# Performance work log

Hardware: AMD Instinct MI355X
Metric: run time of the kernel (lower is better)

The kernel has to match this reference:

```python
import jax, jax.numpy as jnp
import numpy as np

N_CHANNELS = 1024
N_HEADS = 16
SEQ = 2048
BATCH = 2


def setup_inputs() -> dict:
    key = jax.random.key(0)
    k1, k2, k3 = jax.random.split(key, 3)
    x = jax.random.normal(k1, (BATCH, SEQ, N_CHANNELS), dtype=jnp.float32)
    qkv_w = jax.random.normal(k2, (3 * N_CHANNELS, N_CHANNELS), dtype=jnp.float32) * 0.02
    qkv_b = jnp.zeros((3 * N_CHANNELS,), dtype=jnp.float32)
    proj_w = jax.random.normal(k3, (N_CHANNELS, N_CHANNELS), dtype=jnp.float32) * 0.02
    proj_b = jnp.zeros((N_CHANNELS,), dtype=jnp.float32)
    return {"x": x, "qkv_w": qkv_w, "qkv_b": qkv_b, "proj_w": proj_w, "proj_b": proj_b}


def reference(x, qkv_w, qkv_b, proj_w, proj_b):
    bs, t, c = x.shape
    h = N_HEADS
    hd = c // h
    scale = hd ** (-0.5)
    # qkv projection: torch Linear is x @ W^T + b
    qkv = x @ qkv_w.T + qkv_b  # [B, T, 3C]
    qkv = qkv.reshape(bs, t, 3, h, hd)
    q, k, v = qkv[:, :, 0], qkv[:, :, 1], qkv[:, :, 2]  # each [B, T, H, hd]
    logits = jnp.einsum('bthc,bshc->bhts', q, k) * scale  # [B, H, T, T]
    # causal mask: log(tril(ones)) -> 0 below diag, -inf above
    causal = jnp.tril(jnp.ones((t, t), dtype=bool))
    logits = jnp.where(causal[None, None], logits, -jnp.inf)
    attn = jax.nn.softmax(logits, axis=-1)
    out = jnp.einsum('bhts,bshc->bthc', attn, v).reshape(bs, t, c)
    out = out @ proj_w.T + proj_b
    return out
```

## Files before the change

kernel.cpp:

```cpp
#include <hip/hip_runtime.h>

typedef __bf16 bf16x8 __attribute__((ext_vector_type(8)));
typedef float f32x4 __attribute__((ext_vector_type(4)));

__device__ inline ushort f2bf(float f) {
    unsigned u = __builtin_bit_cast(unsigned, f);
    unsigned r = (u + 0x7FFFu + ((u >> 16) & 1u)) >> 16;
    return (ushort)r;
}
__device__ inline float bf2f(ushort u) {
    unsigned x = ((unsigned)u) << 16;
    return __builtin_bit_cast(float, x);
}
__device__ inline uint4 pack8(const float* f) {
    uint4 r;
    r.x = (unsigned)f2bf(f[0]) | ((unsigned)f2bf(f[1]) << 16);
    r.y = (unsigned)f2bf(f[2]) | ((unsigned)f2bf(f[3]) << 16);
    r.z = (unsigned)f2bf(f[4]) | ((unsigned)f2bf(f[5]) << 16);
    r.w = (unsigned)f2bf(f[6]) | ((unsigned)f2bf(f[7]) << 16);
    return r;
}

#define MFMA_BF16(a, b, c) __builtin_amdgcn_mfma_f32_16x16x32_bf16(a, b, c, 0, 0, 0)
#define GLDS(g, l) __builtin_amdgcn_global_load_lds( \
    (const __attribute__((address_space(1))) void*)(g), \
    (__attribute__((address_space(3))) void*)(l), 16, 0, 0)

#define QSCALE 0.18033688011112042f

__global__ __launch_bounds__(256) void convert3(
    const float* __restrict__ s0, ushort* __restrict__ d0,
    const float* __restrict__ s1, ushort* __restrict__ d1,
    const float* __restrict__ s2, ushort* __restrict__ d2)
{
    const int i = blockIdx.x * 256 + threadIdx.x;
    const float* s; ushort* d; int off;
    if (i < 524288)      { s = s0; d = d0; off = i; }
    else if (i < 917504) { s = s1; d = d1; off = i - 524288; }
    else                 { s = s2; d = d2; off = i - 917504; }
    const float4* f = (const float4*)s + off * 2;
    float fa[8];
    *(float4*)&fa[0] = f[0];
    *(float4*)&fa[4] = f[1];
    ((uint4*)d)[off] = pack8(fa);
}

__global__ __launch_bounds__(256) void gemm_qkv(
    const ushort* __restrict__ A, const ushort* __restrict__ B,
    const float* __restrict__ bias,
    ushort* __restrict__ outQ, ushort* __restrict__ outK, ushort* __restrict__ outV,
    int N, int K)
{
    __shared__ __align__(16) ushort SMEM[32768];

    const int tid = threadIdx.x;
    const int w = tid >> 6;
    const int lane = tid & 63;
    const int l15 = lane & 15;
    const int quad = lane >> 4;
    const int srow = lane >> 3;

    const int bid = blockIdx.x + (blockIdx.y << 5);
    const int nb = (bid & 7) * 96 + (bid >> 3);
    const int m0 = (nb / 24) * 128;
    const int n0 = (nb % 24) * 128;
    const int wr = (w & 1) * 64;
    const int wc = (w >> 1) * 64;

    auto stage = [&](int k0, int buf) {
        ushort* As = SMEM + buf * 16384;
        ushort* Bs = As + 8192;
#pragma unroll
        for (int j = 0; j < 4; j++) {
            const int r0 = w * 32 + j * 8;
            const int row = r0 + srow;
            const int gcol = ((lane & 7) ^ (row & 7)) * 8;
            GLDS(A + (size_t)(m0 + row) * K + k0 + gcol, As + r0 * 64);
            GLDS(B + (size_t)(n0 + row) * K + k0 + gcol, Bs + r0 * 64);
        }
    };

    f32x4 acc[4][4] = {};

    stage(0, 0);
    __syncthreads();

    for (int k0 = 0; k0 < K; k0 += 64) {
        const int cur = (k0 >> 6) & 1;
        if (k0 + 64 < K) stage(k0 + 64, cur ^ 1);

        const ushort* As = SMEM + cur * 16384;
        const ushort* Bs = As + 8192;
        bf16x8 af[4][2], bf[4][2];
#pragma unroll
        for (int i = 0; i < 4; i++)
#pragma unroll
            for (int kk = 0; kk < 2; kk++) {
                const int ra = wr + i * 16 + l15;
                const int rb = wc + i * 16 + l15;
                af[i][kk] = *(const bf16x8*)&As[ra * 64 + (((kk * 4 + quad) ^ (ra & 7)) * 8)];
                bf[i][kk] = *(const bf16x8*)&Bs[rb * 64 + (((kk * 4 + quad) ^ (rb & 7)) * 8)];
            }
#pragma unroll
        for (int kk = 0; kk < 2; kk++)
#pragma unroll
            for (int mi = 0; mi < 4; mi++)
#pragma unroll
                for (int ni = 0; ni < 4; ni++)
                    acc[mi][ni] = MFMA_BF16(af[mi][kk], bf[ni][kk], acc[mi][ni]);
        __syncthreads();
    }

    const int which = n0 >> 10;
    ushort* Ct = SMEM;
    if (which == 2) {
#pragma unroll
        for (int mi = 0; mi < 4; mi++)
#pragma unroll
            for (int ni = 0; ni < 4; ni++)
#pragma unroll
                for (int r = 0; r < 4; r++) {
                    const int m_loc = wr + mi * 16 + quad * 4 + r;
                    const int n_loc = wc + ni * 16 + l15;
                    Ct[n_loc * 136 + m_loc] =
                        f2bf(acc[mi][ni][r] + bias[n0 + n_loc]);
                }
        __syncthreads();
        const int b = m0 >> 11;
#pragma unroll
        for (int i = 0; i < 8; i++) {
            const int vi = tid + i * 256;
            const int n_loc = vi >> 4, mblk = vi & 15;
            const uint4 val = *(const uint4*)&Ct[n_loc * 136 + mblk * 8];
            const int t = (m0 & 2047) + mblk * 8;
            const int c = (n0 + n_loc) & 1023;
            const int h = c >> 6, d = c & 63;
            *(uint4*)&outV[((size_t)(b * 16 + h) * 64 + d) * 2048 + t] = val;
        }
    } else {
        const float qs = (which == 0) ? QSCALE : 1.0f;
#pragma unroll
        for (int mi = 0; mi < 4; mi++)
#pragma unroll
            for (int ni = 0; ni < 4; ni++)
#pragma unroll
                for (int r = 0; r < 4; r++) {
                    const int m_loc = wr + mi * 16 + quad * 4 + r;
                    const int n_loc = wc + ni * 16 + l15;
                    Ct[m_loc * 136 + n_loc] =
                        f2bf((acc[mi][ni][r] + bias[n0 + n_loc]) * qs);
                }
        __syncthreads();
        ushort* outP = (which == 0) ? outQ : outK;
        const int hb = (n0 & 1023) >> 6;
        const int b = m0 >> 11;
#pragma unroll
        for (int i = 0; i < 8; i++) {
            const int vi = tid + i * 256;
            const int m_loc = vi >> 4, u = vi & 15;
            const uint4 val = *(const uint4*)&Ct[m_loc * 136 + u * 8];
            const int t = (m0 & 2047) + m_loc;
            const int h = hb + (u >> 3);
            const int d8 = (u & 7) * 8;
            *(uint4*)&outP[((size_t)(b * 16 + h)) * 131072 + (size_t)t * 64 + d8] = val;
        }
    }
}

__global__ __launch_bounds__(256) void gemm_proj(
    const ushort* __restrict__ A, const ushort* __restrict__ B,
    const float* __restrict__ bias, float* __restrict__ outD)
{
    const int N = 1024, K = 1024;
    __shared__ __align__(16) ushort SMEM[24576];

    const int tid = threadIdx.x;
    const int w = tid >> 6;
    const int lane = tid & 63;
    const int l15 = lane & 15;
    const int quad = lane >> 4;
    const int srow = lane >> 3;

    const int bid = blockIdx.x + (blockIdx.y << 6);
    const int nb = (bid & 7) * 64 + (bid >> 3);
    const int m0 = (nb >> 3) * 64;
    const int n0 = (nb & 7) * 128;
    const int wr = (w & 1) * 32;
    const int wc = (w >> 1) * 64;

    auto stage = [&](int k0, int buf) {
        ushort* As = SMEM + buf * 12288;
        ushort* Bs = As + 4096;
#pragma unroll
        for (int j = 0; j < 2; j++) {
            const int r0 = w * 16 + j * 8;
            const int row = r0 + srow;
            const int gcol = ((lane & 7) ^ (row & 7)) * 8;
            GLDS(A + (size_t)(m0 + row) * K + k0 + gcol, As + r0 * 64);
        }
#pragma unroll
        for (int j = 0; j < 4; j++) {
            const int r0 = w * 32 + j * 8;
            const int row = r0 + srow;
            const int gcol = ((lane & 7) ^ (row & 7)) * 8;
            GLDS(B + (size_t)(n0 + row) * K + k0 + gcol, Bs + r0 * 64);
        }
    };

    f32x4 acc[2][4] = {};

    stage(0, 0);
    __syncthreads();

    for (int k0 = 0; k0 < K; k0 += 64) {
        const int cur = (k0 >> 6) & 1;
        if (k0 + 64 < K) stage(k0 + 64, cur ^ 1);

        const ushort* As = SMEM + cur * 12288;
        const ushort* Bs = As + 4096;
        bf16x8 af[2][2], bf[4][2];
#pragma unroll
        for (int kk = 0; kk < 2; kk++) {
#pragma unroll
            for (int mi = 0; mi < 2; mi++) {
                const int ra = wr + mi * 16 + l15;
                af[mi][kk] = *(const bf16x8*)&As[ra * 64 + (((kk * 4 + quad) ^ (ra & 7)) * 8)];
            }
#pragma unroll
            for (int ni = 0; ni < 4; ni++) {
                const int rb = wc + ni * 16 + l15;
                bf[ni][kk] = *(const bf16x8*)&Bs[rb * 64 + (((kk * 4 + quad) ^ (rb & 7)) * 8)];
            }
        }
#pragma unroll
        for (int kk = 0; kk < 2; kk++)
#pragma unroll
            for (int mi = 0; mi < 2; mi++)
#pragma unroll
                for (int ni = 0; ni < 4; ni++)
                    acc[mi][ni] = MFMA_BF16(af[mi][kk], bf[ni][kk], acc[mi][ni]);
        __syncthreads();
    }

    float* Cf = (float*)SMEM;
#pragma unroll
    for (int cch = 0; cch < 2; cch++) {
        __syncthreads();
        if ((wc >> 6) == cch) {
#pragma unroll
            for (int mi = 0; mi < 2; mi++)
#pragma unroll
                for (int ni = 0; ni < 4; ni++)
#pragma unroll
                    for (int r = 0; r < 4; r++) {
                        const int m_loc = wr + mi * 16 + quad * 4 + r;
                        const int nl = ni * 16 + l15;
                        Cf[m_loc * 68 + nl] = acc[mi][ni][r] + bias[n0 + cch * 64 + nl];
                    }
        }
        __syncthreads();
#pragma unroll
        for (int i = 0; i < 4; i++) {
            const int vi = tid + i * 256;
            const int m_loc = vi >> 4, u = vi & 15;
            const float4 val = *(const float4*)&Cf[m_loc * 68 + u * 4];
            *(float4*)&outD[(size_t)(m0 + m_loc) * N + n0 + cch * 64 + u * 4] = val;
        }
    }
}

__global__ __launch_bounds__(256) void attn_split(
    const ushort* __restrict__ Q, const ushort* __restrict__ K,
    const ushort* __restrict__ Vt, ushort* __restrict__ O,
    ushort* __restrict__ Opart, float* __restrict__ Lpart)
{
    __shared__ __align__(16) ushort KV[2][2][64 * 64];
    __shared__ __align__(16) __bf16 Ps[4][16 * 64];

    const int bh = blockIdx.x;
    const int y = blockIdx.y;
    int qt, k0, k1, chunk, split;
    if (y < 48) {
        qt = 31 - (y >> 1); chunk = y & 1; split = 1;
        const int n = qt + 1, h = (n + 1) >> 1;
        k0 = chunk ? h : 0; k1 = chunk ? n : h;
    } else {
        qt = 55 - y; chunk = 0; split = 0; k0 = 0; k1 = qt + 1;
    }
    const int q0 = qt * 64;
    const int tid = threadIdx.x;
    const int w = tid >> 6;
    const int lane = tid & 63;
    const int l15 = lane & 15;
    const int quad = lane >> 4;

    auto stage = [&](int kt, int b) {
        const int t0 = kt * 64;
#pragma unroll
        for (int j = 0; j < 2; j++) {
            const int r0 = w * 16 + j * 8;
            const int row = r0 + (lane >> 3);
            const int gcol = ((lane & 7) ^ (row & 7)) * 8;
            GLDS(K + ((size_t)bh * 2048 + t0 + row) * 64 + gcol, &KV[b][0][r0 * 64]);
            GLDS(Vt + ((size_t)bh * 64 + row) * 2048 + t0 + gcol, &KV[b][1][r0 * 64]);
        }
    };

    const ushort* qbase = Q + ((size_t)bh * 2048 + q0 + w * 16 + l15) * 64;
    bf16x8 qf0 = *(const bf16x8*)(qbase + quad * 8);
    bf16x8 qf1 = *(const bf16x8*)(qbase + 32 + quad * 8);

    bf16x8 ones;
#pragma unroll
    for (int j = 0; j < 8; j++) ones[j] = (__bf16)1.0f;

    f32x4 oacc[4] = {};
    f32x4 lacc = {};

    stage(k0, 0);

    for (int kt = k0; kt < k1; kt++) {
        __syncthreads();
        if (kt + 1 < k1) stage(kt + 1, (kt + 1 - k0) & 1);

        const ushort* Ks = &KV[(kt - k0) & 1][0][0];
        const ushort* Vs = &KV[(kt - k0) & 1][1][0];
        const int t0 = kt * 64;

        f32x4 sacc[4] = {};
#pragma unroll
        for (int cb = 0; cb < 4; cb++) {
            const int rr = cb * 16 + l15;
            bf16x8 b0 = *(const bf16x8*)&Ks[rr * 64 + ((quad ^ (rr & 7)) * 8)];
            bf16x8 b1 = *(const bf16x8*)&Ks[rr * 64 + (((4 + quad) ^ (rr & 7)) * 8)];
            sacc[cb] = MFMA_BF16(qf0, b0, sacc[cb]);
            sacc[cb] = MFMA_BF16(qf1, b1, sacc[cb]);
        }

        __bf16* pw = &Ps[w][0];
        __builtin_amdgcn_wave_barrier();
#pragma unroll
        for (int cb = 0; cb < 4; cb++)
#pragma unroll
            for (int r = 0; r < 4; r++) {
                float x = sacc[cb][r];
                if (kt == qt) {
                    const int col = t0 + cb * 16 + l15;
                    const int row = q0 + w * 16 + quad * 4 + r;
                    if (col > row) x = -1e30f;
                }
                const int prow = quad * 4 + r;
                const int unit = cb * 2 + (l15 >> 3);
                pw[prow * 64 + ((unit ^ (prow & 7)) * 8) + (l15 & 7)] =
                    (__bf16)__builtin_exp2f(x);
            }
        __builtin_amdgcn_s_waitcnt(0xC07F);
        __builtin_amdgcn_wave_barrier();

#pragma unroll
        for (int kc = 0; kc < 2; kc++) {
            bf16x8 afr = *(const bf16x8*)&pw[l15 * 64 + (((kc * 4 + quad) ^ (l15 & 7)) * 8)];
#pragma unroll
            for (int cb = 0; cb < 4; cb++) {
                const int rr = cb * 16 + l15;
                bf16x8 bfr = *(const bf16x8*)&Vs[rr * 64 + (((kc * 4 + quad) ^ (rr & 7)) * 8)];
                oacc[cb] = MFMA_BF16(afr, bfr, oacc[cb]);
            }
            lacc = MFMA_BF16(afr, ones, lacc);
        }
    }

    if (!split) {
        const int b = bh >> 4, h = bh & 15;
#pragma unroll
        for (int r = 0; r < 4; r++) {
            const float inv = 1.0f / lacc[r];
            const int row = q0 + w * 16 + quad * 4 + r;
#pragma unroll
            for (int cb = 0; cb < 4; cb++) {
                const int col = h * 64 + cb * 16 + l15;
                O[((size_t)b * 2048 + row) * 1024 + col] = f2bf(oacc[cb][r] * inv);
            }
        }
    } else {
        const size_t slot2 = ((size_t)bh * 24 + (qt - 8)) * 2 + chunk;
        if (l15 == 0) {
#pragma unroll
            for (int r = 0; r < 4; r++)
                Lpart[slot2 * 64 + w * 16 + quad * 4 + r] = lacc[r];
        }
        __bf16* pw = &Ps[w][0];
        __builtin_amdgcn_wave_barrier();
#pragma unroll
        for (int cb = 0; cb < 4; cb++)
#pragma unroll
            for (int r = 0; r < 4; r++) {
                const int prow = quad * 4 + r;
                const int unit = cb * 2 + (l15 >> 3);
                pw[prow * 64 + ((unit ^ (prow & 7)) * 8) + (l15 & 7)] =
                    (__bf16)oacc[cb][r];
            }
        __builtin_amdgcn_s_waitcnt(0xC07F);
        __builtin_amdgcn_wave_barrier();
        const int r = lane >> 2, u = lane & 3;
        const int p0 = (2 * u) ^ (r & 7), p1 = (2 * u + 1) ^ (r & 7);
        const uint4 a = *(const uint4*)&pw[r * 64 + p0 * 8];
        const uint4 b = *(const uint4*)&pw[r * 64 + p1 * 8];
        ushort* dst = Opart + slot2 * 4096 + (w * 16 + r) * 64 + u * 16;
        *(uint4*)dst = a;
        *(uint4*)(dst + 8) = b;
    }
}

__global__ __launch_bounds__(256) void attn_combine(
    const ushort* __restrict__ Opart, const float* __restrict__ Lpart,
    ushort* __restrict__ O)
{
    const int bh = blockIdx.x;
    const int qt = 8 + blockIdx.y;
    const int tid = threadIdx.x;
    const int row = tid >> 2;
    const int cg = (tid & 3) * 16;
    const size_t s = ((size_t)bh * 24 + (qt - 8)) * 2;
    const ushort* p0 = Opart + s * 4096 + row * 64 + cg;
    const ushort* p1 = p0 + 4096;
    const float inv = 1.0f / (Lpart[s * 64 + row] + Lpart[(s + 1) * 64 + row]);
    const int b = bh >> 4, h = bh & 15;
    ushort* dst = O + ((size_t)b * 2048 + qt * 64 + row) * 1024 + h * 64 + cg;
    ushort out[16];
#pragma unroll
    for (int v = 0; v < 2; v++) {
        uint4 a = *(const uint4*)(p0 + v * 8);
        uint4 c = *(const uint4*)(p1 + v * 8);
        const ushort* ua = (const ushort*)&a;
        const ushort* uc = (const ushort*)&c;
#pragma unroll
        for (int j = 0; j < 8; j++)
            out[v * 8 + j] = f2bf((bf2f(ua[j]) + bf2f(uc[j])) * inv);
    }
    *(uint4*)dst = *(uint4*)&out[0];
    *(uint4*)(dst + 8) = *(uint4*)&out[8];
}

extern "C" void kernel_launch(void* const* d_in, const int* in_sizes, int n_in,
                              void* d_out, int out_size, void* d_ws, size_t ws_size,
                              hipStream_t stream) {
    const float* x      = (const float*)d_in[0];
    const float* qkv_w  = (const float*)d_in[1];
    const float* qkv_b  = (const float*)d_in[2];
    const float* proj_w = (const float*)d_in[3];
    const float* proj_b = (const float*)d_in[4];

    ushort* XbOb  = (ushort*)d_ws + 16;
    ushort* Wqkv  = XbOb + 4194304;
    ushort* Wproj = Wqkv + 3145728;
    ushort* Qb    = Wproj + 1048576;
    ushort* Kb    = Qb + 4194304;
    ushort* Vt    = Kb + 4194304;
    ushort* Opart = Vt + 4194304;
    float*  Lpart = (float*)(Opart + 6291456);

    convert3<<<4096, 256, 0, stream>>>(x, XbOb, qkv_w, Wqkv, proj_w, Wproj);
    gemm_qkv<<<dim3(32, 24), 256, 0, stream>>>(XbOb, Wqkv, qkv_b,
                                               Qb, Kb, Vt, 3072, 1024);
    attn_split<<<dim3(32, 56), 256, 0, stream>>>(Qb, Kb, Vt, XbOb, Opart, Lpart);
    attn_combine<<<dim3(32, 24), 256, 0, stream>>>(Opart, Lpart, XbOb);
    gemm_proj<<<dim3(64, 8), 256, 0, stream>>>(XbOb, Wproj, proj_b, (float*)d_out);
}
```

Measured before the change: 191.2 us.

## Use 128-row query tiles with 32x32 MFMA and register-resident P

Attention now handles 128 query rows per block, with each wave owning 32 rows, and uses 32x32x16 bf16 MFMA computing S^T so that P stays in registers. P is rearranged with v_permlane32_swap instead of a round trip through LDS. Larger query tiles halve the K/V staging traffic per query row and remove the per-wave P shared buffer and its barriers. The trade-offs are fewer blocks (28 per head instead of 56), higher register pressure, and coarser causal load balancing. The split/combine path and Opart layout are resized to match.

```diff
diff --git a/kernel.cpp b/kernel.cpp
--- a/kernel.cpp
+++ b/kernel.cpp
@@ -2,6 +2,7 @@
 
 typedef __bf16 bf16x8 __attribute__((ext_vector_type(8)));
 typedef float f32x4 __attribute__((ext_vector_type(4)));
+typedef float f32x16 __attribute__((ext_vector_type(16)));
 
 __device__ inline ushort f2bf(float f) {
     unsigned u = __builtin_bit_cast(unsigned, f);
@@ -20,8 +21,14 @@
     r.w = (unsigned)f2bf(f[6]) | ((unsigned)f2bf(f[7]) << 16);
     return r;
 }
+__device__ inline unsigned cvtpk_bf16(float lo, float hi) {
+    unsigned r;
+    asm("v_cvt_pk_bf16_f32 %0, %1, %2" : "=v"(r) : "v"(lo), "v"(hi));
+    return r;
+}
 
 #define MFMA_BF16(a, b, c) __builtin_amdgcn_mfma_f32_16x16x32_bf16(a, b, c, 0, 0, 0)
+#define MFMA32(a, b, c) __builtin_amdgcn_mfma_f32_32x32x16_bf16(a, b, c, 0, 0, 0)
 #define GLDS(g, l) __builtin_amdgcn_global_load_lds( \
     (const __attribute__((address_space(1))) void*)(g), \
     (__attribute__((address_space(3))) void*)(l), 16, 0, 0)
@@ -269,30 +276,31 @@
     }
 }
 
-__global__ __launch_bounds__(256) void attn_split(
+__global__ __launch_bounds__(256, 4) void attn_split(
     const ushort* __restrict__ Q, const ushort* __restrict__ K,
     const ushort* __restrict__ Vt, ushort* __restrict__ O,
     ushort* __restrict__ Opart, float* __restrict__ Lpart)
 {
     __shared__ __align__(16) ushort KV[2][2][64 * 64];
-    __shared__ __align__(16) __bf16 Ps[4][16 * 64];
 
     const int bh = blockIdx.x;
     const int y = blockIdx.y;
     int qt, k0, k1, chunk, split;
-    if (y < 48) {
-        qt = 31 - (y >> 1); chunk = y & 1; split = 1;
-        const int n = qt + 1, h = (n + 1) >> 1;
-        k0 = chunk ? h : 0; k1 = chunk ? n : h;
+    if (y < 24) {
+        qt = 15 - (y >> 1); chunk = y & 1; split = 1;
+        const int h2 = qt + 1;
+        k0 = chunk ? h2 : 0; k1 = chunk ? 2 * qt + 2 : h2;
     } else {
-        qt = 55 - y; chunk = 0; split = 0; k0 = 0; k1 = qt + 1;
-    }
-    const int q0 = qt * 64;
+        qt = 27 - y; chunk = 0; split = 0; k0 = 0; k1 = 2 * qt + 2;
+    }
+    const int q0 = qt * 128;
     const int tid = threadIdx.x;
     const int w = tid >> 6;
     const int lane = tid & 63;
-    const int l15 = lane & 15;
-    const int quad = lane >> 4;
+    const int l31 = lane & 31;
+    const int hf = lane >> 5;
+    const int wrow0 = q0 + w * 32;
+    const int rowg = wrow0 + l31;
 
     auto stage = [&](int kt, int b) {
         const int t0 = kt * 64;
@@ -306,16 +314,17 @@
         }
     };
 
-    const ushort* qbase = Q + ((size_t)bh * 2048 + q0 + w * 16 + l15) * 64;
-    bf16x8 qf0 = *(const bf16x8*)(qbase + quad * 8);
-    bf16x8 qf1 = *(const bf16x8*)(qbase + 32 + quad * 8);
+    const ushort* qbase = Q + ((size_t)bh * 2048 + rowg) * 64 + hf * 8;
+    bf16x8 qf[4];
+#pragma unroll
+    for (int db = 0; db < 4; db++) qf[db] = *(const bf16x8*)(qbase + db * 16);
 
     bf16x8 ones;
 #pragma unroll
     for (int j = 0; j < 8; j++) ones[j] = (__bf16)1.0f;
 
-    f32x4 oacc[4] = {};
-    f32x4 lacc = {};
+    f32x16 oacc[2] = {};
+    f32x16 lacc = {};
 
     stage(k0, 0);
 
@@ -327,88 +336,93 @@
         const ushort* Vs = &KV[(kt - k0) & 1][1][0];
         const int t0 = kt * 64;
 
-        f32x4 sacc[4] = {};
-#pragma unroll
-        for (int cb = 0; cb < 4; cb++) {
-            const int rr = cb * 16 + l15;
-            bf16x8 b0 = *(const bf16x8*)&Ks[rr * 64 + ((quad ^ (rr & 7)) * 8)];
-            bf16x8 b1 = *(const bf16x8*)&Ks[rr * 64 + (((4 + quad) ^ (rr & 7)) * 8)];
-            sacc[cb] = MFMA_BF16(qf0, b0, sacc[cb]);
-            sacc[cb] = MFMA_BF16(qf1, b1, sacc[cb]);
-        }
-
-        __bf16* pw = &Ps[w][0];
-        __builtin_amdgcn_wave_barrier();
-#pragma unroll
-        for (int cb = 0; cb < 4; cb++)
-#pragma unroll
-            for (int r = 0; r < 4; r++) {
-                float x = sacc[cb][r];
-                if (kt == qt) {
-                    const int col = t0 + cb * 16 + l15;
-                    const int row = q0 + w * 16 + quad * 4 + r;
-                    if (col > row) x = -1e30f;
-                }
-                const int prow = quad * 4 + r;
-                const int unit = cb * 2 + (l15 >> 3);
-                pw[prow * 64 + ((unit ^ (prow & 7)) * 8) + (l15 & 7)] =
-                    (__bf16)__builtin_exp2f(x);
+        if (t0 <= wrow0 + 31) {
+            f32x16 sacc[2] = {};
+#pragma unroll
+            for (int db = 0; db < 4; db++)
+#pragma unroll
+                for (int kb = 0; kb < 2; kb++) {
+                    const int rr = kb * 32 + l31;
+                    bf16x8 kf = *(const bf16x8*)&Ks[rr * 64 + (((db * 2 + hf) ^ (rr & 7)) * 8)];
+                    sacc[kb] = MFMA32(kf, qf[db], sacc[kb]);
+                }
+
+            unsigned u[2][8];
+            const bool nm = (t0 + 63 > wrow0);
+#pragma unroll
+            for (int kb = 0; kb < 2; kb++) {
+                float p[16];
+                if (nm) {
+#pragma unroll
+                    for (int reg = 0; reg < 16; reg++) {
+                        const int col = t0 + kb * 32 + (reg & 3) + 8 * (reg >> 2) + 4 * hf;
+                        float x = (col > rowg) ? -1e30f : sacc[kb][reg];
+                        p[reg] = __builtin_exp2f(x);
+                    }
+                } else {
+#pragma unroll
+                    for (int reg = 0; reg < 16; reg++)
+                        p[reg] = __builtin_exp2f(sacc[kb][reg]);
+                }
+#pragma unroll
+                for (int t = 0; t < 8; t++)
+                    u[kb][t] = cvtpk_bf16(p[2 * t], p[2 * t + 1]);
             }
-        __builtin_amdgcn_s_waitcnt(0xC07F);
-        __builtin_amdgcn_wave_barrier();
-
-#pragma unroll
-        for (int kc = 0; kc < 2; kc++) {
-            bf16x8 afr = *(const bf16x8*)&pw[l15 * 64 + (((kc * 4 + quad) ^ (l15 & 7)) * 8)];
-#pragma unroll
-            for (int cb = 0; cb < 4; cb++) {
-                const int rr = cb * 16 + l15;
-                bf16x8 bfr = *(const bf16x8*)&Vs[rr * 64 + (((kc * 4 + quad) ^ (rr & 7)) * 8)];
-                oacc[cb] = MFMA_BF16(afr, bfr, oacc[cb]);
+
+#pragma unroll
+            for (int kb = 0; kb < 2; kb++)
+#pragma unroll
+                for (int g = 0; g < 4; g++) {
+                    const int tp = (g & 1) + (g >> 1) * 4;
+                    asm("v_permlane32_swap_b32 %0, %1"
+                        : "+v"(u[kb][tp]), "+v"(u[kb][tp + 2]));
+                }
+
+#pragma unroll
+            for (int m = 0; m < 4; m++) {
+                uint4 av;
+                av.x = u[m >> 1][(m & 1) * 4 + 0];
+                av.y = u[m >> 1][(m & 1) * 4 + 1];
+                av.z = u[m >> 1][(m & 1) * 4 + 2];
+                av.w = u[m >> 1][(m & 1) * 4 + 3];
+                bf16x8 af = __builtin_bit_cast(bf16x8, av);
+                lacc = MFMA32(af, ones, lacc);
+#pragma unroll
+                for (int d2 = 0; d2 < 2; d2++) {
+                    const int rr = d2 * 32 + l31;
+                    bf16x8 vf = *(const bf16x8*)&Vs[rr * 64 + (((m * 2 + hf) ^ (rr & 7)) * 8)];
+                    oacc[d2] = MFMA32(af, vf, oacc[d2]);
+                }
             }
-            lacc = MFMA_BF16(afr, ones, lacc);
         }
     }
 
     if (!split) {
-        const int b = bh >> 4, h = bh & 15;
-#pragma unroll
-        for (int r = 0; r < 4; r++) {
-            const float inv = 1.0f / lacc[r];
-            const int row = q0 + w * 16 + quad * 4 + r;
-#pragma unroll
-            for (int cb = 0; cb < 4; cb++) {
-                const int col = h * 64 + cb * 16 + l15;
-                O[((size_t)b * 2048 + row) * 1024 + col] = f2bf(oacc[cb][r] * inv);
-            }
+        const int b = bh >> 4, hh = bh & 15;
+#pragma unroll
+        for (int reg = 0; reg < 16; reg++) {
+            const int rowf = (reg & 3) + 8 * (reg >> 2) + 4 * hf;
+            const float inv = 1.0f / lacc[reg];
+            const int row = wrow0 + rowf;
+#pragma unroll
+            for (int d2 = 0; d2 < 2; d2++)
+                O[((size_t)b * 2048 + row) * 1024 + hh * 64 + d2 * 32 + l31] =
+                    f2bf(oacc[d2][reg] * inv);
         }
     } else {
-        const size_t slot2 = ((size_t)bh * 24 + (qt - 8)) * 2 + chunk;
-        if (l15 == 0) {
-#pragma unroll
-            for (int r = 0; r < 4; r++)
-                Lpart[slot2 * 64 + w * 16 + quad * 4 + r] = lacc[r];
-        }
-        __bf16* pw = &Ps[w][0];
-        __builtin_amdgcn_wave_barrier();
-#pragma unroll
-        for (int cb = 0; cb < 4; cb++)
-#pragma unroll
-            for (int r = 0; r < 4; r++) {
-                const int prow = quad * 4 + r;
-                const int unit = cb * 2 + (l15 >> 3);
-                pw[prow * 64 + ((unit ^ (prow & 7)) * 8) + (l15 & 7)] =
-                    (__bf16)oacc[cb][r];
-            }
-        __builtin_amdgcn_s_waitcnt(0xC07F);
-        __builtin_amdgcn_wave_barrier();
-        const int r = lane >> 2, u = lane & 3;
-        const int p0 = (2 * u) ^ (r & 7), p1 = (2 * u + 1) ^ (r & 7);
-        const uint4 a = *(const uint4*)&pw[r * 64 + p0 * 8];
-        const uint4 b = *(const uint4*)&pw[r * 64 + p1 * 8];
-        ushort* dst = Opart + slot2 * 4096 + (w * 16 + r) * 64 + u * 16;
-        *(uint4*)dst = a;
-        *(uint4*)(dst + 8) = b;
+        const size_t slot2 = ((size_t)bh * 12 + (qt - 4)) * 2 + chunk;
+        if (l31 == 0) {
+#pragma unroll
+            for (int reg = 0; reg < 16; reg++)
+                Lpart[slot2 * 128 + w * 32 + (reg & 3) + 8 * (reg >> 2) + 4 * hf] = lacc[reg];
+        }
+#pragma unroll
+        for (int reg = 0; reg < 16; reg++) {
+            const int rl = w * 32 + (reg & 3) + 8 * (reg >> 2) + 4 * hf;
+#pragma unroll
+            for (int d2 = 0; d2 < 2; d2++)
+                Opart[slot2 * 8192 + rl * 64 + d2 * 32 + l31] = f2bf(oacc[d2][reg]);
+        }
     }
 }
 
@@ -417,29 +431,28 @@
     ushort* __restrict__ O)
 {
     const int bh = blockIdx.x;
-    const int qt = 8 + blockIdx.y;
+    const int qt = 4 + blockIdx.y;
     const int tid = threadIdx.x;
-    const int row = tid >> 2;
-    const int cg = (tid & 3) * 16;
-    const size_t s = ((size_t)bh * 24 + (qt - 8)) * 2;
-    const ushort* p0 = Opart + s * 4096 + row * 64 + cg;
-    const ushort* p1 = p0 + 4096;
-    const float inv = 1.0f / (Lpart[s * 64 + row] + Lpart[(s + 1) * 64 + row]);
-    const int b = bh >> 4, h = bh & 15;
-    ushort* dst = O + ((size_t)b * 2048 + qt * 64 + row) * 1024 + h * 64 + cg;
-    ushort out[16];
-#pragma unroll
-    for (int v = 0; v < 2; v++) {
+    const int row = tid >> 1;
+    const int dg = (tid & 1) * 32;
+    const size_t s = ((size_t)bh * 12 + (qt - 4)) * 2;
+    const ushort* p0 = Opart + s * 8192 + row * 64 + dg;
+    const ushort* p1 = p0 + 8192;
+    const float inv = 1.0f / (Lpart[s * 128 + row] + Lpart[(s + 1) * 128 + row]);
+    const int b = bh >> 4, hh = bh & 15;
+    ushort* dst = O + ((size_t)b * 2048 + qt * 128 + row) * 1024 + hh * 64 + dg;
+#pragma unroll
+    for (int v = 0; v < 4; v++) {
         uint4 a = *(const uint4*)(p0 + v * 8);
         uint4 c = *(const uint4*)(p1 + v * 8);
         const ushort* ua = (const ushort*)&a;
         const ushort* uc = (const ushort*)&c;
+        ushort out[8];
 #pragma unroll
         for (int j = 0; j < 8; j++)
-            out[v * 8 + j] = f2bf((bf2f(ua[j]) + bf2f(uc[j])) * inv);
-    }
-    *(uint4*)dst = *(uint4*)&out[0];
-    *(uint4*)(dst + 8) = *(uint4*)&out[8];
+            out[j] = f2bf((bf2f(ua[j]) + bf2f(uc[j])) * inv);
+        *(uint4*)(dst + v * 8) = *(uint4*)out;
+    }
 }
 
 extern "C" void kernel_launch(void* const* d_in, const int* in_sizes, int n_in,
@@ -463,7 +476,7 @@
     convert3<<<4096, 256, 0, stream>>>(x, XbOb, qkv_w, Wqkv, proj_w, Wproj);
     gemm_qkv<<<dim3(32, 24), 256, 0, stream>>>(XbOb, Wqkv, qkv_b,
                                                Qb, Kb, Vt, 3072, 1024);
-    attn_split<<<dim3(32, 56), 256, 0, stream>>>(Qb, Kb, Vt, XbOb, Opart, Lpart);
-    attn_combine<<<dim3(32, 24), 256, 0, stream>>>(Opart, Lpart, XbOb);
+    attn_split<<<dim3(32, 28), 256, 0, stream>>>(Qb, Kb, Vt, XbOb, Opart, Lpart);
+    attn_combine<<<dim3(32, 12), 256, 0, stream>>>(Opart, Lpart, XbOb);
     gemm_proj<<<dim3(64, 8), 256, 0, stream>>>(XbOb, Wproj, proj_b, (float*)d_out);
 }
```

New measurement: 209.1 us. 9.3% more time.
